# Kernel tuning notes

Hardware: AMD Instinct MI355X
Metric: run time of the kernel (lower is better)

Reference implementation:

```python
import jax, jax.numpy as jnp
import numpy as np

B, N = 2048, 4096

def setup_inputs() -> dict:
    key = jax.random.key(0)
    k1, k2, k3, k4, k5 = jax.random.split(key, 5)
    scale = 1.0 / np.sqrt(N)  # match nn.Linear init scale
    return {
        "t": jnp.zeros((1,), dtype=jnp.float32),
        "y": jax.random.uniform(k1, (B, N), dtype=jnp.float32),
        "W1": jax.random.normal(k2, (N, N), dtype=jnp.float32) * scale,
        "b1": jax.random.normal(k3, (N,), dtype=jnp.float32) * scale,
        "W2": jax.random.normal(k4, (N, N), dtype=jnp.float32) * scale,
        "b2": jax.random.normal(k5, (N,), dtype=jnp.float32) * scale,
    }

def reference(t, y, W1, b1, W2, b2):
    # out = fcc2(fcc1(y)) : two Linear layers (y @ W^T + b)
    h = y @ W1.T + b1            # [B, N]
    out = h @ W2.T + b2          # [B, N]
    # f = ones(N,1) @ y @ out^T  ==  dot(y, out) broadcast over N;
    # dydt = y * (out - dot(y, out))   (replicator equation)
    dot = jnp.sum(y * out, axis=-1, keepdims=True)  # [B, 1]
    return y * (out - dot)       # [B, N]
```

## Files before the change

### kernel.cpp

```cpp
#include <hip/hip_runtime.h>
#include <hip/hip_bf16.h>
#include <stdint.h>

typedef _Float16 f16;
typedef _Float16 f16x4 __attribute__((ext_vector_type(4)));
typedef _Float16 f16x8 __attribute__((ext_vector_type(8)));
typedef float f32x4 __attribute__((ext_vector_type(4)));

#define ASYNC_COPY16(gsrc, ldst)                                                   \
    __builtin_amdgcn_global_load_lds(                                              \
        (__attribute__((address_space(1))) void*)(gsrc),                           \
        (__attribute__((address_space(3))) void*)(ldst), 16, 0, 0)

#define MFMA16(a, b, c) __builtin_amdgcn_mfma_f32_16x16x32_f16((a), (b), (c), 0, 0, 0)

__global__ __launch_bounds__(256) void cvt_f32_to_f16(const float* __restrict__ in,
                                                      f16* __restrict__ out, int n4) {
    int i = blockIdx.x * 256 + threadIdx.x;
    if (i >= n4) return;
    float4 v = ((const float4*)in)[i];
    f16x4 o;
    o.x = (f16)v.x; o.y = (f16)v.y; o.z = (f16)v.z; o.w = (f16)v.w;
    ((f16x4*)out)[i] = o;
}

__global__ __launch_bounds__(256) void cvt3_f32_to_f16(const float* __restrict__ y,
                                                       const float* __restrict__ W1,
                                                       const float* __restrict__ W2,
                                                       f16* __restrict__ yb,
                                                       f16* __restrict__ w1b,
                                                       f16* __restrict__ w2b,
                                                       int nY4, int nW4) {
    int i = blockIdx.x * 256 + threadIdx.x;
    const float* src;
    f16* dst;
    int off;
    if (i < nY4) {
        src = y; dst = yb; off = i;
    } else if (i < nY4 + nW4) {
        src = W1; dst = w1b; off = i - nY4;
    } else {
        src = W2; dst = w2b; off = i - nY4 - nW4;
        if (off >= nW4) return;
    }
    float4 v = ((const float4*)src)[off];
    f16x4 o;
    o.x = (f16)v.x; o.y = (f16)v.y; o.z = (f16)v.z; o.w = (f16)v.w;
    ((f16x4*)dst)[off] = o;
}

template <int STORE_F16>
__global__ __launch_bounds__(512, 4) void gemm_bt(const f16* __restrict__ A,
                                                  const f16* __restrict__ Bm,
                                                  const float* __restrict__ bias,
                                                  void* __restrict__ Cout,
                                                  int M, int N, int K) {
    constexpr int BM = 128, BN = 128, BK = 64;
    __shared__ __align__(16) f16 sA[2][BM * BK];
    __shared__ __align__(16) f16 sB[2][BN * BK];

    const int tid   = threadIdx.x;
    const int lane  = tid & 63;
    const int wave  = tid >> 6;
    const int waveM = wave >> 2;
    const int waveN = wave & 3;

    const int bm = blockIdx.y * BM;
    const int bn = blockIdx.x * BN;

    const f16* Aptr = A + (size_t)bm * K;
    const f16* Bptr = Bm + (size_t)bn * K;

    const int srow = tid >> 3;
    const int sseg = tid & 7;

    const f16* gA[2];
    const f16* gB[2];
#pragma unroll
    for (int s = 0; s < 2; s++) {
        const int row = s * 64 + srow;
        const int seg = sseg ^ (row & 7);
        gA[s] = Aptr + (size_t)row * K + seg * 8;
        gB[s] = Bptr + (size_t)row * K + seg * 8;
    }
    const int ldst = tid * 8;

#define STAGE_A(s, buf, k0) ASYNC_COPY16(gA[s] + (k0), &sA[buf][(s)*4096 + ldst])
#define STAGE_B(s, buf, k0) ASYNC_COPY16(gB[s] + (k0), &sB[buf][(s)*4096 + ldst])

    f32x4 acc[4][2] = {};

    const int quad = lane >> 4;
    const int l16  = lane & 15;

    const int iters = K / BK;

#pragma unroll
    for (int s = 0; s < 2; s++) STAGE_A(s, 0, 0);
#pragma unroll
    for (int s = 0; s < 2; s++) STAGE_B(s, 0, 0);

    int cur = 0;
    for (int t = 0; t < iters; ++t) {
        __builtin_amdgcn_s_waitcnt(0);
        __syncthreads();

        if (t + 1 < iters) {
            const int k0 = (t + 1) * BK;
#pragma unroll
            for (int s = 0; s < 2; s++) STAGE_A(s, cur ^ 1, k0);
#pragma unroll
            for (int s = 0; s < 2; s++) STAGE_B(s, cur ^ 1, k0);
        }

#pragma unroll
        for (int h = 0; h < 2; h++) {
            f16x8 af[4], bf[2];
#pragma unroll
            for (int mi = 0; mi < 4; mi++) {
                const int row = waveM * 64 + mi * 16 + l16;
                const int seg = (h * 4 + quad) ^ (l16 & 7);
                af[mi] = *(const f16x8*)&sA[cur][row * BK + seg * 8];
            }
#pragma unroll
            for (int ni = 0; ni < 2; ni++) {
                const int row = waveN * 32 + ni * 16 + l16;
                const int seg = (h * 4 + quad) ^ (l16 & 7);
                bf[ni] = *(const f16x8*)&sB[cur][row * BK + seg * 8];
            }
#pragma unroll
            for (int mi = 0; mi < 4; mi++)
#pragma unroll
                for (int ni = 0; ni < 2; ni++)
                    acc[mi][ni] = MFMA16(af[mi], bf[ni], acc[mi][ni]);
        }
        cur ^= 1;
    }

#undef STAGE_A
#undef STAGE_B

#pragma unroll
    for (int ni = 0; ni < 2; ni++) {
        const int col = bn + waveN * 32 + ni * 16 + l16;
        const float bv = bias[col];
#pragma unroll
        for (int mi = 0; mi < 4; mi++) {
            const int row0 = bm + waveM * 64 + mi * 16 + quad * 4;
#pragma unroll
            for (int r = 0; r < 4; r++) {
                float v = acc[mi][ni][r] + bv;
                if (STORE_F16)
                    ((f16*)Cout)[(size_t)(row0 + r) * N + col] = (f16)v;
                else
                    ((float*)Cout)[(size_t)(row0 + r) * N + col] = v;
            }
        }
    }
}

__global__ __launch_bounds__(256) void replicator(const float* __restrict__ y,
                                                  float* __restrict__ out, int N) {
    const int row = blockIdx.x;
    const float4* y4 = (const float4*)(y + (size_t)row * N);
    float4* o4 = (float4*)(out + (size_t)row * N);
    const int n4 = N / 4;

    float p = 0.f;
    for (int i = threadIdx.x; i < n4; i += 256) {
        float4 a = y4[i], b = o4[i];
        p += a.x * b.x + a.y * b.y + a.z * b.z + a.w * b.w;
    }
#pragma unroll
    for (int off = 32; off > 0; off >>= 1) p += __shfl_down(p, off, 64);

    __shared__ float sred[4];
    if ((threadIdx.x & 63) == 0) sred[threadIdx.x >> 6] = p;
    __syncthreads();
    const float dot = sred[0] + sred[1] + sred[2] + sred[3];

    for (int i = threadIdx.x; i < n4; i += 256) {
        float4 a = y4[i], b = o4[i];
        float4 r;
        r.x = a.x * (b.x - dot);
        r.y = a.y * (b.y - dot);
        r.z = a.z * (b.z - dot);
        r.w = a.w * (b.w - dot);
        o4[i] = r;
    }
}

extern "C" void kernel_launch(void* const* d_in, const int* in_sizes, int n_in,
                              void* d_out, int out_size, void* d_ws, size_t ws_size,
                              hipStream_t stream) {
    const float* y  = (const float*)d_in[1];
    const float* W1 = (const float*)d_in[2];
    const float* b1 = (const float*)d_in[3];
    const float* W2 = (const float*)d_in[4];
    const float* b2 = (const float*)d_in[5];

    const int N = in_sizes[3];
    const int B = in_sizes[1] / N;
    float* out = (float*)d_out;

    const size_t szY = (size_t)B * N;
    const size_t szW = (size_t)N * N;

    const int yn4 = (int)(szY / 4);
    const int wn4 = (int)(szW / 4);

    dim3 g1(N / 128, B / 128);

    const size_t need_big = (szY + 2 * szW + szY) * sizeof(f16);

    if (ws_size >= need_big) {
        f16* yb  = (f16*)d_ws;
        f16* w1b = yb + szY;
        f16* w2b = w1b + szW;
        f16* hb  = w2b + szW;

        const int tot4 = yn4 + 2 * wn4;
        cvt3_f32_to_f16<<<(tot4 + 255) / 256, 256, 0, stream>>>(y, W1, W2, yb, w1b, w2b,
                                                                yn4, wn4);
        gemm_bt<1><<<g1, 512, 0, stream>>>(yb, w1b, b1, hb, B, N, N);
        gemm_bt<0><<<g1, 512, 0, stream>>>(hb, w2b, b2, out, B, N, N);
    } else {
        f16* yb = (f16*)d_ws;
        f16* wb = yb + szY;
        f16* hb = wb + szW;

        cvt_f32_to_f16<<<yn4 / 256, 256, 0, stream>>>(y, yb, yn4);
        cvt_f32_to_f16<<<wn4 / 256, 256, 0, stream>>>(W1, wb, wn4);
        gemm_bt<1><<<g1, 512, 0, stream>>>(yb, wb, b1, hb, B, N, N);
        cvt_f32_to_f16<<<wn4 / 256, 256, 0, stream>>>(W2, wb, wn4);
        gemm_bt<0><<<g1, 512, 0, stream>>>(hb, wb, b2, out, B, N, N);
    }

    replicator<<<B, 256, 0, stream>>>(y, out, N);
}
```

Baseline: 353.2 us.

## Load B operand directly from global into registers, drop B shared-memory staging

The GEMM no longer stages the weight (B) tile through LDS. Each wave now reads its B fragments straight from global memory into registers every K-step, and only the A tile stays on the async global-to-LDS double-buffer path. This removes LDS traffic and capacity for B, which could allow higher occupancy. In exchange, B loads are no longer shared across the two waveM waves, so global and L2 traffic for B doubles. The loads are also synchronous and issued right after the barrier, so their latency is exposed before the MFMAs start.

```diff
diff --git a/kernel.cpp b/kernel.cpp
--- a/kernel.cpp
+++ b/kernel.cpp
@@ -55,9 +55,8 @@
                                                   const float* __restrict__ bias,
                                                   void* __restrict__ Cout,
                                                   int M, int N, int K) {
-    constexpr int BM = 128, BN = 128, BK = 64;
+    constexpr int BM = 128, BK = 64;
     __shared__ __align__(16) f16 sA[2][BM * BK];
-    __shared__ __align__(16) f16 sB[2][BN * BK];
 
     const int tid   = threadIdx.x;
     const int lane  = tid & 63;
@@ -66,79 +65,79 @@
     const int waveN = wave & 3;
 
     const int bm = blockIdx.y * BM;
-    const int bn = blockIdx.x * BN;
+    const int bn = blockIdx.x * 128;
 
     const f16* Aptr = A + (size_t)bm * K;
-    const f16* Bptr = Bm + (size_t)bn * K;
 
     const int srow = tid >> 3;
     const int sseg = tid & 7;
 
     const f16* gA[2];
-    const f16* gB[2];
 #pragma unroll
     for (int s = 0; s < 2; s++) {
         const int row = s * 64 + srow;
         const int seg = sseg ^ (row & 7);
         gA[s] = Aptr + (size_t)row * K + seg * 8;
-        gB[s] = Bptr + (size_t)row * K + seg * 8;
     }
     const int ldst = tid * 8;
 
 #define STAGE_A(s, buf, k0) ASYNC_COPY16(gA[s] + (k0), &sA[buf][(s)*4096 + ldst])
-#define STAGE_B(s, buf, k0) ASYNC_COPY16(gB[s] + (k0), &sB[buf][(s)*4096 + ldst])
 
     f32x4 acc[4][2] = {};
 
     const int quad = lane >> 4;
     const int l16  = lane & 15;
 
+    const f16* gB[2];
+#pragma unroll
+    for (int ni = 0; ni < 2; ni++) {
+        const int brow = bn + waveN * 32 + ni * 16 + l16;
+        gB[ni] = Bm + (size_t)brow * K + quad * 8;
+    }
+
     const int iters = K / BK;
 
 #pragma unroll
     for (int s = 0; s < 2; s++) STAGE_A(s, 0, 0);
-#pragma unroll
-    for (int s = 0; s < 2; s++) STAGE_B(s, 0, 0);
 
     int cur = 0;
     for (int t = 0; t < iters; ++t) {
         __builtin_amdgcn_s_waitcnt(0);
         __syncthreads();
 
+        const int k0 = t * BK;
+
+        f16x8 bf[2][2];
+#pragma unroll
+        for (int kh = 0; kh < 2; kh++)
+#pragma unroll
+            for (int ni = 0; ni < 2; ni++)
+                bf[kh][ni] = *(const f16x8*)(gB[ni] + k0 + kh * 32);
+
         if (t + 1 < iters) {
-            const int k0 = (t + 1) * BK;
-#pragma unroll
-            for (int s = 0; s < 2; s++) STAGE_A(s, cur ^ 1, k0);
-#pragma unroll
-            for (int s = 0; s < 2; s++) STAGE_B(s, cur ^ 1, k0);
+#pragma unroll
+            for (int s = 0; s < 2; s++) STAGE_A(s, cur ^ 1, k0 + BK);
         }
 
 #pragma unroll
-        for (int h = 0; h < 2; h++) {
-            f16x8 af[4], bf[2];
+        for (int kh = 0; kh < 2; kh++) {
+            f16x8 af[4];
 #pragma unroll
             for (int mi = 0; mi < 4; mi++) {
                 const int row = waveM * 64 + mi * 16 + l16;
-                const int seg = (h * 4 + quad) ^ (l16 & 7);
+                const int seg = (kh * 4 + quad) ^ (l16 & 7);
                 af[mi] = *(const f16x8*)&sA[cur][row * BK + seg * 8];
             }
 #pragma unroll
-            for (int ni = 0; ni < 2; ni++) {
-                const int row = waveN * 32 + ni * 16 + l16;
-                const int seg = (h * 4 + quad) ^ (l16 & 7);
-                bf[ni] = *(const f16x8*)&sB[cur][row * BK + seg * 8];
-            }
-#pragma unroll
             for (int mi = 0; mi < 4; mi++)
 #pragma unroll
                 for (int ni = 0; ni < 2; ni++)
-                    acc[mi][ni] = MFMA16(af[mi], bf[ni], acc[mi][ni]);
+                    acc[mi][ni] = MFMA16(af[mi], bf[kh][ni], acc[mi][ni]);
         }
         cur ^= 1;
     }
 
 #undef STAGE_A
-#undef STAGE_B
 
 #pragma unroll
     for (int ni = 0; ni < 2; ni++) {
```

After: 479.5 us. 35.8% more time.
